# Performance work log

Measured on AMD Instinct MI355X. Metric: run time of the kernel, lower is better.

The kernel has to match this reference:

```python
import jax, jax.numpy as jnp
import numpy as np

B, IN_DIM, D, C = 16384, 1024, 256, 100


def setup_inputs() -> dict:
    key = jax.random.key(0)
    k1, k2, k3, k4 = jax.random.split(key, 4)
    x = jax.random.normal(k1, (B, IN_DIM), dtype=jnp.float32)
    W = jax.random.normal(k2, (IN_DIM, D), dtype=jnp.float32) * (1.0 / np.sqrt(IN_DIM))
    b = jax.random.normal(k3, (D,), dtype=jnp.float32) * 0.01
    P = jax.random.normal(k4, (C, D), dtype=jnp.float32)  # class prototypes [C, D]
    return {"x": x, "W": W, "b": b, "P": P}


def reference(x, W, b, P):
    # Encoder: Z = x @ W + b  -> [B, D]
    Z = x @ W + b
    d = Z.shape[-1]
    # MSE(r, p) = mean((r - p)^2) = (|r|^2 - 2 r.p + |p|^2) / D
    # Computed via expansion to avoid the [B, C, D] broadcast intermediate.
    sq = (
        jnp.sum(Z * Z, axis=-1, keepdims=True)      # [B, 1]
        - 2.0 * (Z @ P.T)                            # [B, C]
        + jnp.sum(P * P, axis=-1)[None, :]           # [1, C]
    )
    return -sq / d  # [B, C]
```

## Files before the change

### kernel.cpp

```cpp
#include <hip/hip_runtime.h>

#define BATCH 16384
#define KDIM  1024
#define DDIM  256
#define CNUM  100
#define CPAD  112

typedef __bf16 bf16x4 __attribute__((ext_vector_type(4)));
typedef __bf16 bf16x8 __attribute__((ext_vector_type(8)));
typedef float  floatx4 __attribute__((ext_vector_type(4)));

static __device__ __forceinline__ unsigned short f2b(float f) {
    return __builtin_bit_cast(unsigned short, (__bf16)f);
}

static __device__ __forceinline__ void gload_lds16(const unsigned short* g,
                                                   unsigned short* l) {
    __builtin_amdgcn_global_load_lds(
        (const __attribute__((address_space(1))) unsigned int*)g,
        (__attribute__((address_space(3))) unsigned int*)l, 16, 0, 0);
}

__global__ __launch_bounds__(256) void prep(const float* __restrict__ W,
                                            const float* __restrict__ P,
                                            unsigned short* __restrict__ Wt,
                                            unsigned short* __restrict__ Pbf,
                                            float* __restrict__ pnorm2) {
    __shared__ float T[32][33];
    const int bid = blockIdx.x;
    if (bid < 256) {
        const int k0 = (bid & 31) * 32;
        const int n0 = (bid >> 5) * 32;
        const int j  = threadIdx.x & 31;
        const int i0 = threadIdx.x >> 5;
#pragma unroll
        for (int l = 0; l < 4; ++l) {
            int i = i0 + l * 8;
            T[i][j] = W[(k0 + i) * DDIM + n0 + j];
        }
        __syncthreads();
#pragma unroll
        for (int l = 0; l < 4; ++l) {
            int i = i0 + l * 8;
            Wt[(n0 + i) * KDIM + k0 + j] = f2b(T[j][i]);
        }
    } else {
        const int wave = threadIdx.x >> 6;
        const int lane = threadIdx.x & 63;
        const int c = (bid - 256) * 4 + wave;
        float s = 0.f;
#pragma unroll
        for (int jj = 0; jj < 4; ++jj) {
            int d = jj * 64 + lane;
            float v = (c < CNUM) ? P[c * DDIM + d] : 0.f;
            Pbf[c * DDIM + d] = f2b(v);
            s += v * v;
        }
#pragma unroll
        for (int m = 1; m < 64; m <<= 1) s += __shfl_xor(s, m, 64);
        if (lane == 0) pnorm2[c] = s;
    }
}

__global__ __launch_bounds__(256, 8) void fused_main(
    const float* __restrict__ x, const float* __restrict__ bias,
    const unsigned short* __restrict__ Wt, const unsigned short* __restrict__ Pbf,
    const float* __restrict__ pnorm2, float* __restrict__ out)
{
    __shared__ unsigned short U[9216];
    unsigned short* As = U;
    unsigned short* Bs = U + 1024;
    unsigned short* Zs = U;
    __shared__ float rn2[2][32];

    const int tid  = threadIdx.x;
    const int wave = tid >> 6;
    const int lane = tid & 63;
    const int lm   = lane & 15;
    const int lq   = lane >> 4;
    const int rg   = wave >> 1;
    const int ch   = wave & 1;
    const int r0   = blockIdx.x * 32;

    const int rowA = tid >> 3;
    const int kcA  = (tid & 7) * 4;
    const float* gA = x + (r0 + rowA) * KDIM + kcA;

    const unsigned short* gBbase = Wt + (wave * 64 + (lane >> 2)) * KDIM + (lane & 3) * 8;

    floatx4 acc[8];
#pragma unroll
    for (int f = 0; f < 8; ++f) { acc[f][0]=0.f; acc[f][1]=0.f; acc[f][2]=0.f; acc[f][3]=0.f; }

    floatx4 pa = *(const floatx4*)gA;

    for (int kk = 0; kk < KDIM; kk += 32) {
        __syncthreads();
#pragma unroll
        for (int c = 0; c < 4; ++c)
            gload_lds16(gBbase + (c * 16) * KDIM + kk, Bs + (wave * 4 + c) * 512);
        bf16x4 ha;
        ha[0] = (__bf16)pa[0]; ha[1] = (__bf16)pa[1];
        ha[2] = (__bf16)pa[2]; ha[3] = (__bf16)pa[3];
        *(bf16x4*)&As[rowA * 32 + kcA] = ha;
        __syncthreads();
        bf16x8 af = *(const bf16x8*)&As[(rg * 16 + lm) * 32 + lq * 8];
        if (kk + 32 < KDIM)
            pa = *(const floatx4*)(gA + kk + 32);
#pragma unroll
        for (int f = 0; f < 8; ++f) {
            bf16x8 bfr = *(const bf16x8*)&Bs[(ch * 128 + f * 16 + lm) * 32 + lq * 8];
            acc[f] = __builtin_amdgcn_mfma_f32_16x16x32_bf16(af, bfr, acc[f], 0, 0, 0);
        }
    }

#pragma unroll
    for (int f = 0; f < 8; ++f) {
        float bb = bias[ch * 128 + f * 16 + lm];
#pragma unroll
        for (int r = 0; r < 4; ++r) acc[f][r] += bb;
    }

    float s0 = 0.f, s1 = 0.f, s2 = 0.f, s3 = 0.f;
#pragma unroll
    for (int f = 0; f < 8; ++f) {
        s0 += acc[f][0] * acc[f][0];
        s1 += acc[f][1] * acc[f][1];
        s2 += acc[f][2] * acc[f][2];
        s3 += acc[f][3] * acc[f][3];
    }
#pragma unroll
    for (int m = 1; m < 16; m <<= 1) {
        s0 += __shfl_xor(s0, m, 64);
        s1 += __shfl_xor(s1, m, 64);
        s2 += __shfl_xor(s2, m, 64);
        s3 += __shfl_xor(s3, m, 64);
    }
    if (lm == 0) {
        int rl = rg * 16 + lq * 4;
        rn2[ch][rl + 0] = s0;
        rn2[ch][rl + 1] = s1;
        rn2[ch][rl + 2] = s2;
        rn2[ch][rl + 3] = s3;
    }

    __syncthreads();

#pragma unroll
    for (int f = 0; f < 8; ++f) {
        int col = ch * 128 + f * 16 + lm;
#pragma unroll
        for (int r = 0; r < 4; ++r)
            Zs[(rg * 16 + lq * 4 + r) * 264 + col] = f2b(acc[f][r]);
    }
    __syncthreads();

#pragma unroll
    for (int t = 0; t < 2; ++t) {
        const int ct = wave * 2 + t;
        if (ct < 7) {
            floatx4 acc2[2];
#pragma unroll
            for (int nf = 0; nf < 2; ++nf) { acc2[nf][0]=0.f; acc2[nf][1]=0.f; acc2[nf][2]=0.f; acc2[nf][3]=0.f; }
            const unsigned short* gP = Pbf + (ct * 16 + lm) * DDIM + lq * 8;
#pragma unroll
            for (int ks = 0; ks < 8; ++ks) {
                bf16x8 ap = *(const bf16x8*)(gP + ks * 32);
#pragma unroll
                for (int nf = 0; nf < 2; ++nf) {
                    bf16x8 bz = *(const bf16x8*)&Zs[(nf * 16 + lm) * 264 + ks * 32 + lq * 8];
                    acc2[nf] = __builtin_amdgcn_mfma_f32_16x16x32_bf16(ap, bz, acc2[nf], 0, 0, 0);
                }
            }
            int c0 = ct * 16 + lq * 4;
            if (c0 < CNUM) {
                floatx4 pn = *(const floatx4*)(pnorm2 + c0);
#pragma unroll
                for (int nf = 0; nf < 2; ++nf) {
                    int rl = nf * 16 + lm;
                    float rn = rn2[0][rl] + rn2[1][rl];
                    floatx4 o;
#pragma unroll
                    for (int r = 0; r < 4; ++r)
                        o[r] = (2.f * acc2[nf][r] - rn - pn[r]) * (1.f / 256.f);
                    *(floatx4*)&out[(r0 + rl) * CNUM + c0] = o;
                }
            }
        }
    }
}

extern "C" void kernel_launch(void* const* d_in, const int* in_sizes, int n_in,
                              void* d_out, int out_size, void* d_ws, size_t ws_size,
                              hipStream_t stream) {
    const float* x = (const float*)d_in[0];
    const float* W = (const float*)d_in[1];
    const float* b = (const float*)d_in[2];
    const float* P = (const float*)d_in[3];
    float* out = (float*)d_out;

    unsigned short* Wt  = (unsigned short*)d_ws;
    unsigned short* Pbf = Wt + KDIM * DDIM;
    float* pn2 = (float*)(Pbf + CPAD * DDIM);

    prep<<<256 + CPAD / 4, 256, 0, stream>>>(W, P, Wt, Pbf, pn2);
    fused_main<<<BATCH / 32, 256, 0, stream>>>(x, b, Wt, Pbf, pn2, out);
}
```

Measured before the change: 134.1 us.

## Double K-step to 64 with XOR-swizzled LDS and per-wave column tiling

Each block iteration now covers 64 K elements instead of 32, halving the number of barrier pairs per block. LDS tiles for A and B use an XOR swizzle to avoid bank conflicts. Waves are re-tiled so each owns 64 output columns across both 16-row groups, reusing each B fragment for two MFMAs. The row-norm reduction now combines four per-wave partials. LDS use doubles and the occupancy hint drops from 8 to 4 blocks, which may reduce latency hiding.

```diff
diff --git a/kernel.cpp b/kernel.cpp
--- a/kernel.cpp
+++ b/kernel.cpp
@@ -62,97 +62,122 @@
     }
 }
 
-__global__ __launch_bounds__(256, 8) void fused_main(
+__global__ __launch_bounds__(256, 4) void fused_main(
     const float* __restrict__ x, const float* __restrict__ bias,
     const unsigned short* __restrict__ Wt, const unsigned short* __restrict__ Pbf,
     const float* __restrict__ pnorm2, float* __restrict__ out)
 {
-    __shared__ unsigned short U[9216];
+    __shared__ unsigned short U[18432];
     unsigned short* As = U;
-    unsigned short* Bs = U + 1024;
+    unsigned short* Bs = U + 2048;
     unsigned short* Zs = U;
-    __shared__ float rn2[2][32];
+    __shared__ float rn2[4][32];
 
     const int tid  = threadIdx.x;
     const int wave = tid >> 6;
     const int lane = tid & 63;
     const int lm   = lane & 15;
     const int lq   = lane >> 4;
-    const int rg   = wave >> 1;
-    const int ch   = wave & 1;
     const int r0   = blockIdx.x * 32;
 
     const int rowA = tid >> 3;
-    const int kcA  = (tid & 7) * 4;
-    const float* gA = x + (r0 + rowA) * KDIM + kcA;
-
-    const unsigned short* gBbase = Wt + (wave * 64 + (lane >> 2)) * KDIM + (lane & 3) * 8;
-
-    floatx4 acc[8];
-#pragma unroll
-    for (int f = 0; f < 8; ++f) { acc[f][0]=0.f; acc[f][1]=0.f; acc[f][2]=0.f; acc[f][3]=0.f; }
-
-    floatx4 pa = *(const floatx4*)gA;
-
-    for (int kk = 0; kk < KDIM; kk += 32) {
+    const int kbA  = tid & 7;
+    const float* gA = x + (r0 + rowA) * KDIM + kbA * 8;
+    const int ldsA = rowA * 64 + ((kbA ^ (rowA & 7)) * 8);
+
+    const int gkb = (lane & 7) ^ ((lane >> 3) & 7);
+    const unsigned short* gB = Wt + (wave * 64 + (lane >> 3)) * KDIM + gkb * 8;
+    unsigned short* ldsB = Bs + (wave * 64) * 64;
+
+    const int sw0 = ((0 * 4 + lq) ^ (lm & 7)) * 8;
+    const int sw1 = ((1 * 4 + lq) ^ (lm & 7)) * 8;
+
+    floatx4 acc[2][4];
+#pragma unroll
+    for (int g = 0; g < 2; ++g)
+#pragma unroll
+        for (int f = 0; f < 4; ++f) { acc[g][f][0]=0.f; acc[g][f][1]=0.f; acc[g][f][2]=0.f; acc[g][f][3]=0.f; }
+
+    floatx4 pa0 = *(const floatx4*)(gA);
+    floatx4 pa1 = *(const floatx4*)(gA + 4);
+
+#pragma unroll 2
+    for (int kk = 0; kk < KDIM; kk += 64) {
         __syncthreads();
 #pragma unroll
-        for (int c = 0; c < 4; ++c)
-            gload_lds16(gBbase + (c * 16) * KDIM + kk, Bs + (wave * 4 + c) * 512);
-        bf16x4 ha;
-        ha[0] = (__bf16)pa[0]; ha[1] = (__bf16)pa[1];
-        ha[2] = (__bf16)pa[2]; ha[3] = (__bf16)pa[3];
-        *(bf16x4*)&As[rowA * 32 + kcA] = ha;
+        for (int j = 0; j < 8; ++j)
+            gload_lds16(gB + j * 8 * KDIM + kk, ldsB + j * 8 * 64);
+        bf16x8 ha;
+        ha[0] = (__bf16)pa0[0]; ha[1] = (__bf16)pa0[1];
+        ha[2] = (__bf16)pa0[2]; ha[3] = (__bf16)pa0[3];
+        ha[4] = (__bf16)pa1[0]; ha[5] = (__bf16)pa1[1];
+        ha[6] = (__bf16)pa1[2]; ha[7] = (__bf16)pa1[3];
+        *(bf16x8*)&As[ldsA] = ha;
         __syncthreads();
-        bf16x8 af = *(const bf16x8*)&As[(rg * 16 + lm) * 32 + lq * 8];
-        if (kk + 32 < KDIM)
-            pa = *(const floatx4*)(gA + kk + 32);
-#pragma unroll
-        for (int f = 0; f < 8; ++f) {
-            bf16x8 bfr = *(const bf16x8*)&Bs[(ch * 128 + f * 16 + lm) * 32 + lq * 8];
-            acc[f] = __builtin_amdgcn_mfma_f32_16x16x32_bf16(af, bfr, acc[f], 0, 0, 0);
-        }
-    }
-
-#pragma unroll
-    for (int f = 0; f < 8; ++f) {
-        float bb = bias[ch * 128 + f * 16 + lm];
-#pragma unroll
-        for (int r = 0; r < 4; ++r) acc[f][r] += bb;
-    }
-
-    float s0 = 0.f, s1 = 0.f, s2 = 0.f, s3 = 0.f;
-#pragma unroll
-    for (int f = 0; f < 8; ++f) {
-        s0 += acc[f][0] * acc[f][0];
-        s1 += acc[f][1] * acc[f][1];
-        s2 += acc[f][2] * acc[f][2];
-        s3 += acc[f][3] * acc[f][3];
-    }
-#pragma unroll
-    for (int m = 1; m < 16; m <<= 1) {
-        s0 += __shfl_xor(s0, m, 64);
-        s1 += __shfl_xor(s1, m, 64);
-        s2 += __shfl_xor(s2, m, 64);
-        s3 += __shfl_xor(s3, m, 64);
-    }
-    if (lm == 0) {
-        int rl = rg * 16 + lq * 4;
-        rn2[ch][rl + 0] = s0;
-        rn2[ch][rl + 1] = s1;
-        rn2[ch][rl + 2] = s2;
-        rn2[ch][rl + 3] = s3;
+        if (kk + 64 < KDIM) {
+            pa0 = *(const floatx4*)(gA + kk + 64);
+            pa1 = *(const floatx4*)(gA + kk + 68);
+        }
+#pragma unroll
+        for (int kf = 0; kf < 2; ++kf) {
+            const int sw = kf ? sw1 : sw0;
+            bf16x8 a0 = *(const bf16x8*)&As[lm * 64 + sw];
+            bf16x8 a1 = *(const bf16x8*)&As[(16 + lm) * 64 + sw];
+#pragma unroll
+            for (int f = 0; f < 4; ++f) {
+                bf16x8 bfr = *(const bf16x8*)&Bs[(wave * 64 + f * 16 + lm) * 64 + sw];
+                acc[0][f] = __builtin_amdgcn_mfma_f32_16x16x32_bf16(a0, bfr, acc[0][f], 0, 0, 0);
+                acc[1][f] = __builtin_amdgcn_mfma_f32_16x16x32_bf16(a1, bfr, acc[1][f], 0, 0, 0);
+            }
+        }
+    }
+
+#pragma unroll
+    for (int f = 0; f < 4; ++f) {
+        float bb = bias[wave * 64 + f * 16 + lm];
+#pragma unroll
+        for (int g = 0; g < 2; ++g)
+#pragma unroll
+            for (int r = 0; r < 4; ++r) acc[g][f][r] += bb;
+    }
+
+#pragma unroll
+    for (int g = 0; g < 2; ++g) {
+        float s0 = 0.f, s1 = 0.f, s2 = 0.f, s3 = 0.f;
+#pragma unroll
+        for (int f = 0; f < 4; ++f) {
+            s0 += acc[g][f][0] * acc[g][f][0];
+            s1 += acc[g][f][1] * acc[g][f][1];
+            s2 += acc[g][f][2] * acc[g][f][2];
+            s3 += acc[g][f][3] * acc[g][f][3];
+        }
+#pragma unroll
+        for (int m = 1; m < 16; m <<= 1) {
+            s0 += __shfl_xor(s0, m, 64);
+            s1 += __shfl_xor(s1, m, 64);
+            s2 += __shfl_xor(s2, m, 64);
+            s3 += __shfl_xor(s3, m, 64);
+        }
+        if (lm == 0) {
+            int rl = g * 16 + lq * 4;
+            rn2[wave][rl + 0] = s0;
+            rn2[wave][rl + 1] = s1;
+            rn2[wave][rl + 2] = s2;
+            rn2[wave][rl + 3] = s3;
+        }
     }
 
     __syncthreads();
 
 #pragma unroll
-    for (int f = 0; f < 8; ++f) {
-        int col = ch * 128 + f * 16 + lm;
-#pragma unroll
-        for (int r = 0; r < 4; ++r)
-            Zs[(rg * 16 + lq * 4 + r) * 264 + col] = f2b(acc[f][r]);
-    }
+    for (int g = 0; g < 2; ++g)
+#pragma unroll
+        for (int f = 0; f < 4; ++f) {
+            int col = wave * 64 + f * 16 + lm;
+#pragma unroll
+            for (int r = 0; r < 4; ++r)
+                Zs[(g * 16 + lq * 4 + r) * 264 + col] = f2b(acc[g][f][r]);
+        }
     __syncthreads();
 
 #pragma unroll
@@ -178,7 +203,7 @@
 #pragma unroll
                 for (int nf = 0; nf < 2; ++nf) {
                     int rl = nf * 16 + lm;
-                    float rn = rn2[0][rl] + rn2[1][rl];
+                    float rn = rn2[0][rl] + rn2[1][rl] + rn2[2][rl] + rn2[3][rl];
                     floatx4 o;
 #pragma unroll
                     for (int r = 0; r < 4; ++r)
```

New measurement: 124.1 us. -7.5%, faster.
